# Performance work log

Hardware: AMD Instinct MI355X
Metric: run time of the kernel (lower is better)

The kernel has to match this reference:

```python
import jax, jax.numpy as jnp
import numpy as np

B, S, T = 4, 512, 512
D, F, L, H, V = 512, 2048, 6, 8, 32000
HD = D // H


def setup_inputs() -> dict:
    key = jax.random.key(0)
    ks = list(jax.random.split(key, 16))
    it = iter(ks)

    def w(shape, scale=0.02):
        return jax.random.normal(next(it), shape, jnp.float32) * scale

    enc_in = jax.random.randint(next(it), (B, S), 0, V, dtype=jnp.int32)
    dec_in = jax.random.randint(next(it), (B, T), 0, V, dtype=jnp.int32)

    # sinusoidal positional encoding (make_sine_pos_encoding)
    pos = np.arange(S)[:, None].astype(np.float32)
    i = np.arange(D)[None, :].astype(np.float32)
    angle = pos / np.power(10000.0, (2.0 * np.floor(i / 2.0)) / D)
    pe = np.zeros((S, D), np.float32)
    pe[:, 0::2] = np.sin(angle[:, 0::2])
    pe[:, 1::2] = np.cos(angle[:, 1::2])

    return {
        "enc_in": enc_in,
        "dec_in": dec_in,
        "e_embed": w((V, D)),
        "d_embed": w((V, D)),
        "pos_enc": jnp.asarray(pe),
        "enc_mha_W": w((L, 4, D, D)),      # q,k,v,out
        "enc_mha_b": jnp.zeros((L, 4, D), jnp.float32),
        "enc_ln_g": jnp.ones((L, 2, D), jnp.float32),
        "enc_ln_b": jnp.zeros((L, 2, D), jnp.float32),
        "enc_ffn_W1": w((L, D, F)),
        "enc_ffn_b1": jnp.zeros((L, F), jnp.float32),
        "enc_ffn_W2": w((L, F, D)),
        "enc_ffn_b2": jnp.zeros((L, D), jnp.float32),
        "dec_mha_W": w((L, 8, D, D)),      # self q,k,v,out then cross q,k,v,out
        "dec_mha_b": jnp.zeros((L, 8, D), jnp.float32),
        "dec_ln_g": jnp.ones((L, 3, D), jnp.float32),
        "dec_ln_b": jnp.zeros((L, 3, D), jnp.float32),
        "dec_ffn_W1": w((L, D, F)),
        "dec_ffn_b1": jnp.zeros((L, F), jnp.float32),
        "dec_ffn_W2": w((L, F, D)),
        "dec_ffn_b2": jnp.zeros((L, D), jnp.float32),
    }


def _layer_norm(x, g, b, eps=1e-6):
    m = jnp.mean(x, axis=-1, keepdims=True)
    v = jnp.mean(jnp.square(x - m), axis=-1, keepdims=True)
    return (x - m) * jax.lax.rsqrt(v + eps) * g + b


def _split_heads(x):
    b, n, _ = x.shape
    return x.reshape(b, n, H, HD).transpose(0, 2, 1, 3)  # b h n d


def _mha(xq, xkv, W, b, mask):
    # W: [>=4, D, D] slice of (q,k,v,out); mask: broadcastable to [b,h,nq,nk]
    q = _split_heads(xq @ W[0] + b[0])
    k = _split_heads(xkv @ W[1] + b[1])
    v = _split_heads(xkv @ W[2] + b[2])
    s = jnp.einsum('bhqd,bhkd->bhqk', q, k) / jnp.sqrt(jnp.float32(HD))
    s = s + mask * (-1e9)
    a = jax.nn.softmax(s, axis=-1)
    o = jnp.einsum('bhqk,bhkd->bhqd', a, v)
    o = o.transpose(0, 2, 1, 3).reshape(xq.shape[0], xq.shape[1], D)
    return o @ W[3] + b[3]


def _forward(enc_in, dec_in, e_embed, d_embed, pos_enc,
             enc_mha_W, enc_mha_b, enc_ln_g, enc_ln_b,
             enc_ffn_W1, enc_ffn_b1, enc_ffn_W2, enc_ffn_b2,
             dec_mha_W, dec_mha_b, dec_ln_g, dec_ln_b,
             dec_ffn_W1, dec_ffn_b1, dec_ffn_W2, dec_ffn_b2):
    # masks: 1.0 where attention is blocked
    enc_pad = (enc_in == 0).astype(jnp.float32)[:, None, None, :]   # [B,1,1,S]
    dec_pad = (dec_in == 0).astype(jnp.float32)[:, None, None, :]   # [B,1,1,T]
    la = jnp.triu(jnp.ones((T, T), jnp.float32), k=1)[None, None]   # [1,1,T,T]
    look_ahead = jnp.maximum(la, dec_pad)                           # [B,1,T,T]

    scale = jnp.float32(D) ** 0.5
    e = e_embed[enc_in] * scale + pos_enc[None, :S]
    d = d_embed[dec_in] * scale + pos_enc[None, :T]

    for l in range(L):
        y = _mha(e, e, enc_mha_W[l], enc_mha_b[l], enc_pad)
        e = _layer_norm(e + y, enc_ln_g[l, 0], enc_ln_b[l, 0])
        y = jax.nn.relu(e @ enc_ffn_W1[l] + enc_ffn_b1[l]) @ enc_ffn_W2[l] + enc_ffn_b2[l]
        e = _layer_norm(e + y, enc_ln_g[l, 1], enc_ln_b[l, 1])

    for l in range(L):
        y = _mha(d, d, dec_mha_W[l, 0:4], dec_mha_b[l, 0:4], look_ahead)
        d = _layer_norm(d + y, dec_ln_g[l, 0], dec_ln_b[l, 0])
        y = _mha(d, e, dec_mha_W[l, 4:8], dec_mha_b[l, 4:8], enc_pad)
        d = _layer_norm(d + y, dec_ln_g[l, 1], dec_ln_b[l, 1])
        y = jax.nn.relu(d @ dec_ffn_W1[l] + dec_ffn_b1[l]) @ dec_ffn_W2[l] + dec_ffn_b2[l]
        d = _layer_norm(d + y, dec_ln_g[l, 2], dec_ln_b[l, 2])

    return d @ d_embed.T  # [B,T,V] logits


def reference(enc_in, dec_in, e_embed, d_embed, pos_enc,
              enc_mha_W, enc_mha_b, enc_ln_g, enc_ln_b,
              enc_ffn_W1, enc_ffn_b1, enc_ffn_W2, enc_ffn_b2,
              dec_mha_W, dec_mha_b, dec_ln_g, dec_ln_b,
              dec_ffn_W1, dec_ffn_b1, dec_ffn_W2, dec_ffn_b2):
    return _forward(enc_in, dec_in, e_embed, d_embed, pos_enc,
                    enc_mha_W, enc_mha_b, enc_ln_g, enc_ln_b,
                    enc_ffn_W1, enc_ffn_b1, enc_ffn_W2, enc_ffn_b2,
                    dec_mha_W, dec_mha_b, dec_ln_g, dec_ln_b,
                    dec_ffn_W1, dec_ffn_b1, dec_ffn_W2, dec_ffn_b2)
```

## Files before the change

### kernel.cpp

```cpp
#include <hip/hip_runtime.h>
#include <hip/hip_bf16.h>
#include <math.h>

#define B_ 4
#define S_ 512
#define D_ 512
#define F_ 2048
#define L_ 6
#define H_ 8
#define V_ 32000

typedef unsigned short u16;
typedef __attribute__((ext_vector_type(8))) short bhalf8;
typedef __attribute__((ext_vector_type(4))) float f32x4;

__device__ __forceinline__ u16 f2b(float v) {
    unsigned x = __builtin_bit_cast(unsigned, v);
    return (u16)((x + 0x7FFFu + ((x >> 16) & 1u)) >> 16);
}

#define GLD16(g, l) __builtin_amdgcn_global_load_lds( \
    (const __attribute__((address_space(1))) void*)(g), \
    (__attribute__((address_space(3))) void*)(l), 16, 0, 0)

__device__ __forceinline__ float redmax16(float v) {
    #pragma unroll
    for (int m = 1; m < 16; m <<= 1) v = fmaxf(v, __shfl_xor(v, m));
    return v;
}
__device__ __forceinline__ float redsum16(float v) {
    #pragma unroll
    for (int m = 1; m < 16; m <<= 1) v += __shfl_xor(v, m);
    return v;
}

template<int NWR, int NWC, int WM, int WN, int OUT, int RELU, int MLOOP,
         int SPLITA, int XMAJOR, int NT, int VTT>
__global__ __launch_bounds__(NWR * NWC * 64)
void mfma_gemm(const u16* __restrict__ A, const u16* __restrict__ A2, int acut,
               const u16* __restrict__ B,
               const float* __restrict__ bias, void* __restrict__ Cv,
               int K, int lda, int ldb, int ldc,
               u16* __restrict__ vtp, int vc0)
{
    constexpr int BM = NWR * WM, BN = NWC * WN;
    constexpr int NW = NWR * NWC;
    constexpr int CH_A = BM / 16, CH_B = BN / 16, CH = CH_A + CH_B;
    constexpr int NI = WM / 16, NJ = WN / 16;

    __shared__ u16 As[BM * 32];
    __shared__ u16 Bs[BN * 32];
    __shared__ u16 TT[VTT ? 64 * 72 : 8];

    const int tid = threadIdx.x;
    const int wid = tid >> 6, lane = tid & 63;
    const int wrow = wid / NWC, wcol = wid % NWC;
    const long bn = (XMAJOR ? (long)blockIdx.y : (long)blockIdx.x) * BN;
    const long bmbase = (XMAJOR ? (long)blockIdx.x : (long)blockIdx.y);
    const int r4 = lane >> 2, c4 = lane & 3;
    const int l15 = lane & 15, l4 = lane >> 4;

    const u16* Ause = (SPLITA && bn >= acut) ? A2 : A;

    #pragma unroll 1
    for (int mi = 0; mi < MLOOP; ++mi) {
        const long bm = (bmbase * MLOOP + mi) * BM;

        f32x4 acc[NI][NJ];
        #pragma unroll
        for (int i = 0; i < NI; ++i)
            #pragma unroll
            for (int j = 0; j < NJ; ++j)
                acc[i][j] = (f32x4){0.f, 0.f, 0.f, 0.f};

        for (int k0 = 0; k0 < K; k0 += 32) {
            #pragma unroll
            for (int t = 0; t < CH / NW; ++t) {
                int c = wid + t * NW;
                if (c < CH_A) {
                    const u16* g = Ause + (bm + c * 16 + r4) * (long)lda + k0 + c4 * 8;
                    GLD16(g, As + c * 512 + lane * 8);
                } else {
                    int cb = c - CH_A;
                    const u16* g = B + (bn + cb * 16 + r4) * (long)ldb + k0 + c4 * 8;
                    GLD16(g, Bs + cb * 512 + lane * 8);
                }
            }
            __syncthreads();
            bhalf8 af[NI], bfr[NJ];
            #pragma unroll
            for (int i = 0; i < NI; ++i)
                af[i] = *(const bhalf8*)&As[(wrow * WM + i * 16 + l15) * 32 + l4 * 8];
            #pragma unroll
            for (int j = 0; j < NJ; ++j)
                bfr[j] = *(const bhalf8*)&Bs[(wcol * WN + j * 16 + l15) * 32 + l4 * 8];
            #pragma unroll
            for (int i = 0; i < NI; ++i)
                #pragma unroll
                for (int j = 0; j < NJ; ++j)
                    acc[i][j] = __builtin_amdgcn_mfma_f32_16x16x32_bf16(af[i], bfr[j], acc[i][j], 0, 0, 0);
            __syncthreads();
        }

        if (VTT && vtp != nullptr && bn >= vc0) {
            #pragma unroll
            for (int j = 0; j < NJ; ++j) {
                const int c = wcol * WN + j * 16 + l15;
                const float bv = bias ? bias[bn + c] : 0.f;
                #pragma unroll
                for (int i = 0; i < NI; ++i) {
                    const int rw = wrow * WM + i * 16 + (l4 << 2);
                    #pragma unroll
                    for (int r = 0; r < 4; ++r)
                        TT[c * 72 + rw + r] = f2b(acc[i][j][r] + bv);
                }
            }
            __syncthreads();
            {
                const int c = tid >> 1, hh = tid & 1;
                const u16* src = &TT[c * 72 + hh * 32];
                u16* dst = &vtp[(bn - vc0 + c) * 2048 + bm + hh * 32];
                #pragma unroll
                for (int p = 0; p < 4; ++p)
                    *(uint4*)(dst + p * 8) = *(const uint4*)(src + p * 8);
            }
            __syncthreads();
            continue;
        }

        float* Cf = (float*)Cv;
        u16*   Cb = (u16*)Cv;
        const int rowb = wrow * WM + (l4 << 2);
        const int colb = wcol * WN + l15;
        #pragma unroll
        for (int j = 0; j < NJ; ++j) {
            const long gc = bn + colb + j * 16;
            const float bv = bias ? bias[gc] : 0.f;
            #pragma unroll
            for (int i = 0; i < NI; ++i) {
                const long gr = bm + rowb + i * 16;
                #pragma unroll
                for (int r = 0; r < 4; ++r) {
                    float v = acc[i][j][r] + bv;
                    if (RELU) v = fmaxf(v, 0.f);
                    if (OUT == 0) {
                        if (NT) __builtin_nontemporal_store(v, &Cf[(gr + r) * (long)ldc + gc]);
                        else    Cf[(gr + r) * (long)ldc + gc] = v;
                    } else {
                        Cb[(gr + r) * (long)ldc + gc] = f2b(v);
                    }
                }
            }
        }
    }
}

__global__ __launch_bounds__(512)
void gemm_ln_kernel(const u16* __restrict__ A, const u16* __restrict__ B,
                    const float* __restrict__ bias,
                    float* __restrict__ x, u16* __restrict__ xb,
                    const float* __restrict__ g, const float* __restrict__ bb,
                    int K)
{
    __shared__ u16 As[16 * 32];
    __shared__ u16 Bs[512 * 32];
    __shared__ float red[2][16][8];
    __shared__ float mv[2][16];

    const int tid = threadIdx.x, w = tid >> 6, lane = tid & 63;
    const int l15 = lane & 15, l4 = lane >> 4;
    const int r4 = lane >> 2, c4 = lane & 3;
    const long bm = (long)blockIdx.x * 16;

    f32x4 acc[4];
    #pragma unroll
    for (int j = 0; j < 4; ++j) acc[j] = (f32x4){0.f, 0.f, 0.f, 0.f};

    for (int k0 = 0; k0 < K; k0 += 32) {
        #pragma unroll
        for (int t = 0; t < 5; ++t) {
            int c = w + t * 8;
            if (c < 33) {
                if (c == 0) {
                    GLD16(A + (bm + r4) * (long)K + k0 + c4 * 8, As + lane * 8);
                } else {
                    GLD16(B + ((c - 1) * 16 + r4) * (long)K + k0 + c4 * 8,
                          Bs + (c - 1) * 512 + lane * 8);
                }
            }
        }
        __syncthreads();
        bhalf8 af = *(const bhalf8*)&As[l15 * 32 + l4 * 8];
        #pragma unroll
        for (int j = 0; j < 4; ++j) {
            bhalf8 bf = *(const bhalf8*)&Bs[(w * 64 + j * 16 + l15) * 32 + l4 * 8];
            acc[j] = __builtin_amdgcn_mfma_f32_16x16x32_bf16(af, bf, acc[j], 0, 0, 0);
        }
        __syncthreads();
    }

    float vbuf[4][4], s[4] = {0, 0, 0, 0}, s2[4] = {0, 0, 0, 0};
    #pragma unroll
    for (int j = 0; j < 4; ++j) {
        int col = w * 64 + j * 16 + l15;
        float bv = bias[col];
        #pragma unroll
        for (int r = 0; r < 4; ++r) {
            int row = l4 * 4 + r;
            float v = acc[j][r] + bv + x[(bm + row) * 512 + col];
            vbuf[j][r] = v;
            s[r] += v; s2[r] += v * v;
        }
    }
    #pragma unroll
    for (int r = 0; r < 4; ++r) { s[r] = redsum16(s[r]); s2[r] = redsum16(s2[r]); }
    if (l15 == 0) {
        #pragma unroll
        for (int r = 0; r < 4; ++r) {
            red[0][l4 * 4 + r][w] = s[r];
            red[1][l4 * 4 + r][w] = s2[r];
        }
    }
    __syncthreads();
    if (tid < 16) {
        float S = 0.f, S2 = 0.f;
        #pragma unroll
        for (int q = 0; q < 8; ++q) { S += red[0][tid][q]; S2 += red[1][tid][q]; }
        float mean = S * (1.f / 512.f);
        float var = S2 * (1.f / 512.f) - mean * mean;
        mv[0][tid] = mean;
        mv[1][tid] = rsqrtf(var + 1e-6f);
    }
    __syncthreads();
    #pragma unroll
    for (int j = 0; j < 4; ++j) {
        int col = w * 64 + j * 16 + l15;
        float gg = g[col], bbv = bb[col];
        #pragma unroll
        for (int r = 0; r < 4; ++r) {
            int row = l4 * 4 + r;
            float o = (vbuf[j][r] - mv[0][row]) * mv[1][row] * gg + bbv;
            x[(bm + row) * 512 + col] = o;
            xb[(bm + row) * 512 + col] = f2b(o);
        }
    }
}

template<int CAUSAL>
__global__ __launch_bounds__(256)
void flash_kernel(const u16* __restrict__ Qp, int ldq,
                  const u16* __restrict__ Kp, int ldk,
                  const u16* __restrict__ Vt,
                  const int* __restrict__ tok,
                  u16* __restrict__ Op)
{
    __shared__ u16 QS[64 * 64];
    __shared__ u16 KS[64 * 64];
    __shared__ u16 VS[64 * 64];
    __shared__ u16 PS[4 * 16 * 64];
    __shared__ float MK[512];

    const int tid = threadIdx.x, lane = tid & 63, w = tid >> 6;
    const int l15 = lane & 15, l4 = lane >> 4;
    const int qb = blockIdx.x, bh = blockIdx.y;
    const int b = bh >> 3, h = bh & 7;

    const u16* Q = Qp + (long)(b * 512 + qb * 64) * ldq + h * 64;
    const u16* K = Kp + (long)(b * 512) * ldk + h * 64;
    const u16* V = Vt + (long)(h * 64) * 2048 + b * 512;
    u16* O = Op + (long)(b * 512 + qb * 64) * 512 + h * 64;

    {
        int t0 = tok[b * 512 + tid];
        int t1 = tok[b * 512 + 256 + tid];
        MK[tid]       = (t0 == 0) ? -1e9f : 0.f;
        MK[tid + 256] = (t1 == 0) ? -1e9f : 0.f;
    }
    {
        int r = tid >> 3;
        int c = (tid & 7) ^ (r & 7);
        GLD16(Q + (long)r * ldq + c * 8,        QS + tid * 8);
        GLD16(Q + (long)(r + 32) * ldq + c * 8, QS + 2048 + tid * 8);
    }

    f32x4 oacc[4];
    float mrun[4], lrun[4];
    #pragma unroll
    for (int j = 0; j < 4; ++j) oacc[j] = (f32x4){0.f, 0.f, 0.f, 0.f};
    #pragma unroll
    for (int r = 0; r < 4; ++r) { mrun[r] = -1e30f; lrun[r] = 0.f; }

    bhalf8 qa[2];
    const int tmax = CAUSAL ? qb : 7;

    for (int t = 0; t <= tmax; ++t) {
        {
            int r = tid >> 3;
            int c = (tid & 7) ^ (r & 7);
            GLD16(K + (long)(t * 64 + r) * ldk + c * 8,       KS + tid * 8);
            GLD16(K + (long)(t * 64 + 32 + r) * ldk + c * 8,  KS + 2048 + tid * 8);
            GLD16(V + (long)r * 2048 + t * 64 + c * 8,        VS + tid * 8);
            GLD16(V + (long)(r + 32) * 2048 + t * 64 + c * 8, VS + 2048 + tid * 8);
        }
        __syncthreads();
        if (t == 0) {
            #pragma unroll
            for (int kc = 0; kc < 2; ++kc) {
                int row = w * 16 + l15;
                qa[kc] = *(const bhalf8*)&QS[row * 64 + (((kc * 4 + l4) ^ (row & 7)) << 3)];
            }
        }
        f32x4 sac[4];
        #pragma unroll
        for (int jj = 0; jj < 4; ++jj) sac[jj] = (f32x4){0.f, 0.f, 0.f, 0.f};
        bhalf8 kf[4][2];
        #pragma unroll
        for (int jj = 0; jj < 4; ++jj)
            #pragma unroll
            for (int kc = 0; kc < 2; ++kc) {
                int row = jj * 16 + l15;
                kf[jj][kc] = *(const bhalf8*)&KS[row * 64 + (((kc * 4 + l4) ^ (row & 7)) << 3)];
            }
        #pragma unroll
        for (int jj = 0; jj < 4; ++jj)
            #pragma unroll
            for (int kc = 0; kc < 2; ++kc)
                sac[jj] = __builtin_amdgcn_mfma_f32_16x16x32_bf16(qa[kc], kf[jj][kc], sac[jj], 0, 0, 0);

        #pragma unroll
        for (int jj = 0; jj < 4; ++jj) {
            float mk = MK[t * 64 + jj * 16 + l15];
            #pragma unroll
            for (int r = 0; r < 4; ++r) {
                float mk2 = mk;
                if (CAUSAL && t == qb) {
                    int col = t * 64 + jj * 16 + l15;
                    int qr = qb * 64 + w * 16 + l4 * 4 + r;
                    if (col > qr) mk2 = -1e9f;
                }
                sac[jj][r] = sac[jj][r] * 0.125f + mk2;
            }
        }
        #pragma unroll
        for (int r = 0; r < 4; ++r) {
            float mx = fmaxf(fmaxf(sac[0][r], sac[1][r]), fmaxf(sac[2][r], sac[3][r]));
            mx = redmax16(mx);
            float mnew = fmaxf(mrun[r], mx);
            float alpha = __expf(mrun[r] - mnew);
            float sum = 0.f;
            int row_p = l4 * 4 + r;
            #pragma unroll
            for (int jj = 0; jj < 4; ++jj) {
                float pv = __expf(sac[jj][r] - mnew);
                sum += pv;
                int kv = jj * 16 + l15;
                PS[w * 1024 + row_p * 64 + ((((kv >> 3) ^ (row_p & 7)) << 3) | (kv & 7))] = f2b(pv);
            }
            sum = redsum16(sum);
            lrun[r] = lrun[r] * alpha + sum;
            mrun[r] = mnew;
            #pragma unroll
            for (int jd = 0; jd < 4; ++jd) oacc[jd][r] *= alpha;
        }
        bhalf8 pa[2], vf[4][2];
        #pragma unroll
        for (int kc = 0; kc < 2; ++kc) {
            int row = l15;
            pa[kc] = *(const bhalf8*)&PS[w * 1024 + row * 64 + (((kc * 4 + l4) ^ (row & 7)) << 3)];
        }
        #pragma unroll
        for (int jd = 0; jd < 4; ++jd)
            #pragma unroll
            for (int kc = 0; kc < 2; ++kc) {
                int row = jd * 16 + l15;
                vf[jd][kc] = *(const bhalf8*)&VS[row * 64 + (((kc * 4 + l4) ^ (row & 7)) << 3)];
            }
        #pragma unroll
        for (int jd = 0; jd < 4; ++jd)
            #pragma unroll
            for (int kc = 0; kc < 2; ++kc)
                oacc[jd] = __builtin_amdgcn_mfma_f32_16x16x32_bf16(pa[kc], vf[jd][kc], oacc[jd], 0, 0, 0);
        __syncthreads();
    }

    #pragma unroll
    for (int r = 0; r < 4; ++r) {
        float inv = 1.f / lrun[r];
        int row = w * 16 + l4 * 4 + r;
        #pragma unroll
        for (int jd = 0; jd < 4; ++jd)
            O[(long)row * 512 + jd * 16 + l15] = f2b(oacc[jd][r] * inv);
    }
}

__global__ __launch_bounds__(256)
void transpose_many(const float* __restrict__ inA, const float* __restrict__ inB,
                    int zsplit, int R, int C, u16* __restrict__ out)
{
    int z = blockIdx.z;
    const float* in = (z < zsplit) ? inA + (long)z * R * C
                                   : inB + (long)(z - zsplit) * R * C;
    u16* o = out + (long)z * R * C;
    __shared__ float tb[64][65];
    const int tr = blockIdx.y * 64, tc = blockIdx.x * 64;
    const int col = threadIdx.x & 63, r0 = threadIdx.x >> 6;
    #pragma unroll
    for (int p = 0; p < 16; ++p) {
        int row = r0 * 16 + p;
        tb[row][col] = in[(long)(tr + row) * C + tc + col];
    }
    __syncthreads();
    #pragma unroll
    for (int p = 0; p < 16; ++p) {
        int row = r0 * 16 + p;
        o[(long)(tc + row) * R + tr + col] = f2b(tb[col][row]);
    }
}

__global__ __launch_bounds__(256)
void convert_b16(const float4* __restrict__ in, u16* __restrict__ out, long n4)
{
    long i = (long)blockIdx.x * 256 + threadIdx.x;
    if (i >= n4) return;
    float4 v = in[i];
    uint2 p;
    p.x = (unsigned)f2b(v.x) | ((unsigned)f2b(v.y) << 16);
    p.y = (unsigned)f2b(v.z) | ((unsigned)f2b(v.w) << 16);
    *(uint2*)(out + i * 4) = p;
}

__global__ __launch_bounds__(256)
void embed_kernel(const int* __restrict__ tE, const int* __restrict__ tD,
                  const float* __restrict__ eE, const float* __restrict__ eD,
                  const float* __restrict__ pos,
                  float* __restrict__ xE, float* __restrict__ xD,
                  u16* __restrict__ bE, u16* __restrict__ bD, float scale)
{
    const int z = blockIdx.y;
    const int* tok = z ? tD : tE;
    const float* emb = z ? eD : eE;
    float* x = z ? xD : xE;
    u16* xb = z ? bD : bE;
    int row = blockIdx.x;
    int s = row & (S_ - 1);
    int t = tok[row];
    const float* er = emb + (long)t * D_;
    const float* pr = pos + (long)s * D_;
    float* o = x + (long)row * D_;
    u16*  ob = xb + (long)row * D_;
    int i = threadIdx.x;
    float v0 = er[i]       * scale + pr[i];
    float v1 = er[i + 256] * scale + pr[i + 256];
    o[i] = v0;        o[i + 256] = v1;
    ob[i] = f2b(v0);  ob[i + 256] = f2b(v1);
}

__global__ __launch_bounds__(256)
void add_ln_kernel(float* __restrict__ x, const float* __restrict__ y,
                   u16* __restrict__ xb,
                   const float* __restrict__ g, const float* __restrict__ bb)
{
    long row = blockIdx.x;
    float* xr = x + row * D_;
    u16* xo = xb + row * D_;
    const float* yr = y + row * D_;
    int t = threadIdx.x, t2 = t + 256;

    float r0 = xr[t] + yr[t];
    float r1 = xr[t2] + yr[t2];
    float s = r0 + r1;
    float s2 = r0 * r0 + r1 * r1;
    #pragma unroll
    for (int i = 1; i < 64; i <<= 1) {
        s  += __shfl_xor(s, i);
        s2 += __shfl_xor(s2, i);
    }
    __shared__ float rs[4], rs2[4];
    int wid = t >> 6;
    if ((t & 63) == 0) { rs[wid] = s; rs2[wid] = s2; }
    __syncthreads();
    s  = rs[0] + rs[1] + rs[2] + rs[3];
    s2 = rs2[0] + rs2[1] + rs2[2] + rs2[3];

    float mean = s * (1.f / D_);
    float var  = s2 * (1.f / D_) - mean * mean;
    float inv  = rsqrtf(var + 1e-6f);
    float o0 = (r0 - mean) * inv * g[t]  + bb[t];
    float o1 = (r1 - mean) * inv * g[t2] + bb[t2];
    xr[t] = o0;       xr[t2] = o1;
    xo[t] = f2b(o0);  xo[t2] = f2b(o1);
}

extern "C" void kernel_launch(void* const* d_in, const int* in_sizes, int n_in,
                              void* d_out, int out_size, void* d_ws, size_t ws_size,
                              hipStream_t stream)
{
    const int*   enc_in     = (const int*)  d_in[0];
    const int*   dec_in     = (const int*)  d_in[1];
    const float* e_embed    = (const float*)d_in[2];
    const float* d_embed    = (const float*)d_in[3];
    const float* pos_enc    = (const float*)d_in[4];
    const float* enc_mha_W  = (const float*)d_in[5];
    const float* enc_mha_b  = (const float*)d_in[6];
    const float* enc_ln_g   = (const float*)d_in[7];
    const float* enc_ln_b   = (const float*)d_in[8];
    const float* enc_ffn_W1 = (const float*)d_in[9];
    const float* enc_ffn_b1 = (const float*)d_in[10];
    const float* enc_ffn_W2 = (const float*)d_in[11];
    const float* enc_ffn_b2 = (const float*)d_in[12];
    const float* dec_mha_W  = (const float*)d_in[13];
    const float* dec_mha_b  = (const float*)d_in[14];
    const float* dec_ln_g   = (const float*)d_in[15];
    const float* dec_ln_b   = (const float*)d_in[16];
    const float* dec_ffn_W1 = (const float*)d_in[17];
    const float* dec_ffn_b1 = (const float*)d_in[18];
    const float* dec_ffn_W2 = (const float*)d_in[19];
    const float* dec_ffn_b2 = (const float*)d_in[20];
    float* out = (float*)d_out;

    const int  BS  = B_ * S_;
    const long BSD = (long)BS * D_;
    const long DD  = (long)D_ * D_;
    const long DF  = (long)D_ * F_;

    char* p = (char*)d_ws;
    auto alloc = [&](long bytes) { char* r = p; p += (bytes + 255) & ~255L; return r; };
    float* e    = (float*)alloc(BSD * 4);
    float* dd   = (float*)alloc(BSD * 4);
    float* y    = (float*)alloc(BSD * 4);
    u16*   eb   = (u16*)  alloc(BSD * 2);
    u16*   ddb  = (u16*)  alloc(BSD * 2);
    u16*   qkv  = (u16*)  alloc((long)BS * 1536 * 2);
    u16*   att  = (u16*)  alloc(BSD * 2);
    u16*   vt   = (u16*)  alloc(BSD * 2);
    u16*   ffnh = (u16*)  alloc((long)BS * F_ * 2);
    u16*   wEmb = (u16*)  alloc((long)V_ * D_ * 2);
    u16*   wMha = (u16*)  alloc(72 * DD * 2);
    u16*   wF1  = (u16*)  alloc(12 * DF * 2);
    u16*   wF2  = (u16*)  alloc(12 * DF * 2);

    transpose_many<<<dim3(8, 8, 72), 256, 0, stream>>>(enc_mha_W, dec_mha_W, 24, 512, 512, wMha);
    transpose_many<<<dim3(32, 8, 12), 256, 0, stream>>>(enc_ffn_W1, dec_ffn_W1, 6, 512, 2048, wF1);
    transpose_many<<<dim3(8, 32, 12), 256, 0, stream>>>(enc_ffn_W2, dec_ffn_W2, 6, 2048, 512, wF2);
    convert_b16<<<16000, 256, 0, stream>>>((const float4*)d_embed, wEmb, (long)V_ * D_ / 4);

    const float scale = sqrtf((float)D_);
    embed_kernel<<<dim3(BS, 2), 256, 0, stream>>>(enc_in, dec_in, e_embed, d_embed,
                                                  pos_enc, e, dd, eb, ddb, scale);

    #define GEMM_BIG(grid, RELU, OUTT, A, Bp, bias, C, K, lda, ldb, ldc) \
        mfma_gemm<2,2,64,64,OUTT,RELU,1,0,0,0,0><<<grid, 256, 0, stream>>>(A, A, 1 << 30, Bp, bias, C, K, lda, ldb, ldc, nullptr, 0)
    #define GEMM_SKV(grid, A, Bp, bias, C, K, lda, ldb, ldc, vtp, vc0) \
        mfma_gemm<2,1,32,64,1,0,1,0,0,0,1><<<grid, 128, 0, stream>>>(A, A, 1 << 30, Bp, bias, C, K, lda, ldb, ldc, vtp, vc0)
    #define GEMM_SK(grid, OUTT, A, Bp, bias, C, K, lda, ldb, ldc) \
        mfma_gemm<2,1,32,64,OUTT,0,1,0,0,0,0><<<grid, 128, 0, stream>>>(A, A, 1 << 30, Bp, bias, C, K, lda, ldb, ldc, nullptr, 0)

    for (int l = 0; l < L_; ++l) {
        const u16* Wl = wMha + (long)l * 4 * DD;
        const float* bl = enc_mha_b + (long)l * 4 * D_;
        GEMM_SKV(dim3(24, 32), eb, Wl, bl, qkv, 512, 512, 512, 1536, vt, 1024);
        flash_kernel<0><<<dim3(8, 32), 256, 0, stream>>>(qkv, 1536, qkv + 512, 1536, vt, enc_in, att);
        gemm_ln_kernel<<<128, 512, 0, stream>>>(att, Wl + 3 * DD, bl + 3 * D_,
            e, eb, enc_ln_g + (long)(l * 2) * D_, enc_ln_b + (long)(l * 2) * D_, 512);
        GEMM_BIG(dim3(16, 16), 1, 1, eb, wF1 + (long)l * DF, enc_ffn_b1 + (long)l * F_,
                 ffnh, 512, 512, 512, 2048);
        GEMM_SK(dim3(8, 32), 0, ffnh, wF2 + (long)l * DF, enc_ffn_b2 + (long)l * D_,
                y, 2048, 2048, 2048, 512);
        add_ln_kernel<<<BS, 256, 0, stream>>>(e, y, eb,
            enc_ln_g + (long)(l * 2 + 1) * D_, enc_ln_b + (long)(l * 2 + 1) * D_);
    }

    for (int l = 0; l < L_; ++l) {
        const u16* Wl = wMha + (long)(24 + l * 8) * DD;
        const float* bl = dec_mha_b + (long)l * 8 * D_;
        GEMM_SKV(dim3(24, 32), ddb, Wl, bl, qkv, 512, 512, 512, 1536, vt, 1024);
        flash_kernel<1><<<dim3(8, 32), 256, 0, stream>>>(qkv, 1536, qkv + 512, 1536, vt, dec_in, att);
        gemm_ln_kernel<<<128, 512, 0, stream>>>(att, Wl + 3 * DD, bl + 3 * D_,
            dd, ddb, dec_ln_g + (long)(l * 3) * D_, dec_ln_b + (long)(l * 3) * D_, 512);
        mfma_gemm<2,1,32,64,1,0,1,1,0,0,1><<<dim3(24, 32), 128, 0, stream>>>(
            ddb, eb, 512, Wl + 4 * DD, bl + 4 * D_, qkv,
            512, 512, 512, 1536, vt, 1024);
        flash_kernel<0><<<dim3(8, 32), 256, 0, stream>>>(qkv, 1536, qkv + 512, 1536, vt, enc_in, att);
        gemm_ln_kernel<<<128, 512, 0, stream>>>(att, Wl + 7 * DD, bl + 7 * D_,
            dd, ddb, dec_ln_g + (long)(l * 3 + 1) * D_, dec_ln_b + (long)(l * 3 + 1) * D_, 512);
        GEMM_BIG(dim3(16, 16), 1, 1, ddb, wF1 + (long)(6 + l) * DF, dec_ffn_b1 + (long)l * F_,
                 ffnh, 512, 512, 512, 2048);
        GEMM_SK(dim3(8, 32), 0, ffnh, wF2 + (long)(6 + l) * DF, dec_ffn_b2 + (long)l * D_,
                y, 2048, 2048, 2048, 512);
        add_ln_kernel<<<BS, 256, 0, stream>>>(dd, y, ddb,
            dec_ln_g + (long)(l * 3 + 2) * D_, dec_ln_b + (long)(l * 3 + 2) * D_);
    }

    mfma_gemm<2,2,64,64,0,0,1,0,1,1,0><<<dim3(16, 250), 256, 0, stream>>>(
        ddb, ddb, 1 << 30, wEmb, nullptr, out, 512, 512, 512, 32000, nullptr, 0);
}
```

Before: 1.805 ms.

## Fuse FFN2 with add+LayerNorm, halve flash query tile, swizzle logits grid

Three separate changes. The second FFN GEMM now goes through the existing gemm_ln_kernel with K=2048, which folds bias, residual add and LayerNorm into one kernel and drops the fp32 y buffer and the separate add_ln launch. The flash attention kernel now handles 32-query tiles with 128 threads, doubling the grid to 512 blocks for better occupancy and finer causal work balance. The final vocab-projection GEMM uses a 1D grid with an XCD-aware swizzle so blocks sharing B tiles land on the same chiplet. In exchange, the fused LN GEMM runs only 128 blocks over a K=2048 loop, and the smaller flash tiles reload K/V more often.

```diff
diff --git a/kernel.cpp b/kernel.cpp
--- a/kernel.cpp
+++ b/kernel.cpp
@@ -35,7 +35,7 @@
 }
 
 template<int NWR, int NWC, int WM, int WN, int OUT, int RELU, int MLOOP,
-         int SPLITA, int XMAJOR, int NT, int VTT>
+         int SPLITA, int XMAJOR, int NT, int VTT, int SWZ>
 __global__ __launch_bounds__(NWR * NWC * 64)
 void mfma_gemm(const u16* __restrict__ A, const u16* __restrict__ A2, int acut,
                const u16* __restrict__ B,
@@ -55,8 +55,17 @@
     const int tid = threadIdx.x;
     const int wid = tid >> 6, lane = tid & 63;
     const int wrow = wid / NWC, wcol = wid % NWC;
-    const long bn = (XMAJOR ? (long)blockIdx.y : (long)blockIdx.x) * BN;
-    const long bmbase = (XMAJOR ? (long)blockIdx.x : (long)blockIdx.y);
+    long bn, bmbase;
+    if (SWZ) {
+        long b0 = blockIdx.x;
+        long per = (long)gridDim.x >> 3;
+        long w = (b0 & 7) * per + (b0 >> 3);
+        bn = (w >> 4) * BN;
+        bmbase = w & 15;
+    } else {
+        bn = (XMAJOR ? (long)blockIdx.y : (long)blockIdx.x) * BN;
+        bmbase = (XMAJOR ? (long)blockIdx.x : (long)blockIdx.y);
+    }
     const int r4 = lane >> 2, c4 = lane & 3;
     const int l15 = lane & 15, l4 = lane >> 4;
 
@@ -247,17 +256,17 @@
 }
 
 template<int CAUSAL>
-__global__ __launch_bounds__(256)
+__global__ __launch_bounds__(128)
 void flash_kernel(const u16* __restrict__ Qp, int ldq,
                   const u16* __restrict__ Kp, int ldk,
                   const u16* __restrict__ Vt,
                   const int* __restrict__ tok,
                   u16* __restrict__ Op)
 {
-    __shared__ u16 QS[64 * 64];
+    __shared__ u16 QS[32 * 64];
     __shared__ u16 KS[64 * 64];
     __shared__ u16 VS[64 * 64];
-    __shared__ u16 PS[4 * 16 * 64];
+    __shared__ u16 PS[2 * 16 * 64];
     __shared__ float MK[512];
 
     const int tid = threadIdx.x, lane = tid & 63, w = tid >> 6;
@@ -265,22 +274,21 @@
     const int qb = blockIdx.x, bh = blockIdx.y;
     const int b = bh >> 3, h = bh & 7;
 
-    const u16* Q = Qp + (long)(b * 512 + qb * 64) * ldq + h * 64;
+    const u16* Q = Qp + (long)(b * 512 + qb * 32) * ldq + h * 64;
     const u16* K = Kp + (long)(b * 512) * ldk + h * 64;
     const u16* V = Vt + (long)(h * 64) * 2048 + b * 512;
-    u16* O = Op + (long)(b * 512 + qb * 64) * 512 + h * 64;
-
-    {
-        int t0 = tok[b * 512 + tid];
-        int t1 = tok[b * 512 + 256 + tid];
-        MK[tid]       = (t0 == 0) ? -1e9f : 0.f;
-        MK[tid + 256] = (t1 == 0) ? -1e9f : 0.f;
+    u16* O = Op + (long)(b * 512 + qb * 32) * 512 + h * 64;
+
+    #pragma unroll
+    for (int t = 0; t < 4; ++t) {
+        int tk = tok[b * 512 + t * 128 + tid];
+        MK[t * 128 + tid] = (tk == 0) ? -1e9f : 0.f;
     }
     {
         int r = tid >> 3;
         int c = (tid & 7) ^ (r & 7);
-        GLD16(Q + (long)r * ldq + c * 8,        QS + tid * 8);
-        GLD16(Q + (long)(r + 32) * ldq + c * 8, QS + 2048 + tid * 8);
+        GLD16(Q + (long)r * ldq + c * 8,          QS + tid * 8);
+        GLD16(Q + (long)(16 + r) * ldq + c * 8,   QS + 1024 + tid * 8);
     }
 
     f32x4 oacc[4];
@@ -291,16 +299,20 @@
     for (int r = 0; r < 4; ++r) { mrun[r] = -1e30f; lrun[r] = 0.f; }
 
     bhalf8 qa[2];
-    const int tmax = CAUSAL ? qb : 7;
+    const int tmax = CAUSAL ? (qb >> 1) : 7;
 
     for (int t = 0; t <= tmax; ++t) {
         {
             int r = tid >> 3;
             int c = (tid & 7) ^ (r & 7);
             GLD16(K + (long)(t * 64 + r) * ldk + c * 8,       KS + tid * 8);
+            GLD16(K + (long)(t * 64 + 16 + r) * ldk + c * 8,  KS + 1024 + tid * 8);
             GLD16(K + (long)(t * 64 + 32 + r) * ldk + c * 8,  KS + 2048 + tid * 8);
+            GLD16(K + (long)(t * 64 + 48 + r) * ldk + c * 8,  KS + 3072 + tid * 8);
             GLD16(V + (long)r * 2048 + t * 64 + c * 8,        VS + tid * 8);
-            GLD16(V + (long)(r + 32) * 2048 + t * 64 + c * 8, VS + 2048 + tid * 8);
+            GLD16(V + (long)(16 + r) * 2048 + t * 64 + c * 8, VS + 1024 + tid * 8);
+            GLD16(V + (long)(32 + r) * 2048 + t * 64 + c * 8, VS + 2048 + tid * 8);
+            GLD16(V + (long)(48 + r) * 2048 + t * 64 + c * 8, VS + 3072 + tid * 8);
         }
         __syncthreads();
         if (t == 0) {
@@ -333,9 +345,9 @@
             #pragma unroll
             for (int r = 0; r < 4; ++r) {
                 float mk2 = mk;
-                if (CAUSAL && t == qb) {
+                if (CAUSAL && t == tmax) {
                     int col = t * 64 + jj * 16 + l15;
-                    int qr = qb * 64 + w * 16 + l4 * 4 + r;
+                    int qr = qb * 32 + w * 16 + l4 * 4 + r;
                     if (col > qr) mk2 = -1e9f;
                 }
                 sac[jj][r] = sac[jj][r] * 0.125f + mk2;
@@ -453,42 +465,6 @@
     float v1 = er[i + 256] * scale + pr[i + 256];
     o[i] = v0;        o[i + 256] = v1;
     ob[i] = f2b(v0);  ob[i + 256] = f2b(v1);
-}
-
-__global__ __launch_bounds__(256)
-void add_ln_kernel(float* __restrict__ x, const float* __restrict__ y,
-                   u16* __restrict__ xb,
-                   const float* __restrict__ g, const float* __restrict__ bb)
-{
-    long row = blockIdx.x;
-    float* xr = x + row * D_;
-    u16* xo = xb + row * D_;
-    const float* yr = y + row * D_;
-    int t = threadIdx.x, t2 = t + 256;
-
-    float r0 = xr[t] + yr[t];
-    float r1 = xr[t2] + yr[t2];
-    float s = r0 + r1;
-    float s2 = r0 * r0 + r1 * r1;
-    #pragma unroll
-    for (int i = 1; i < 64; i <<= 1) {
-        s  += __shfl_xor(s, i);
-        s2 += __shfl_xor(s2, i);
-    }
-    __shared__ float rs[4], rs2[4];
-    int wid = t >> 6;
-    if ((t & 63) == 0) { rs[wid] = s; rs2[wid] = s2; }
-    __syncthreads();
-    s  = rs[0] + rs[1] + rs[2] + rs[3];
-    s2 = rs2[0] + rs2[1] + rs2[2] + rs2[3];
-
-    float mean = s * (1.f / D_);
-    float var  = s2 * (1.f / D_) - mean * mean;
-    float inv  = rsqrtf(var + 1e-6f);
-    float o0 = (r0 - mean) * inv * g[t]  + bb[t];
-    float o1 = (r1 - mean) * inv * g[t2] + bb[t2];
-    xr[t] = o0;       xr[t2] = o1;
-    xo[t] = f2b(o0);  xo[t2] = f2b(o1);
 }
 
 extern "C" void kernel_launch(void* const* d_in, const int* in_sizes, int n_in,
@@ -527,7 +503,6 @@
     auto alloc = [&](long bytes) { char* r = p; p += (bytes + 255) & ~255L; return r; };
     float* e    = (float*)alloc(BSD * 4);
     float* dd   = (float*)alloc(BSD * 4);
-    float* y    = (float*)alloc(BSD * 4);
     u16*   eb   = (u16*)  alloc(BSD * 2);
     u16*   ddb  = (u16*)  alloc(BSD * 2);
     u16*   qkv  = (u16*)  alloc((long)BS * 1536 * 2);
@@ -549,48 +524,42 @@
                                                   pos_enc, e, dd, eb, ddb, scale);
 
     #define GEMM_BIG(grid, RELU, OUTT, A, Bp, bias, C, K, lda, ldb, ldc) \
-        mfma_gemm<2,2,64,64,OUTT,RELU,1,0,0,0,0><<<grid, 256, 0, stream>>>(A, A, 1 << 30, Bp, bias, C, K, lda, ldb, ldc, nullptr, 0)
+        mfma_gemm<2,2,64,64,OUTT,RELU,1,0,0,0,0,0><<<grid, 256, 0, stream>>>(A, A, 1 << 30, Bp, bias, C, K, lda, ldb, ldc, nullptr, 0)
     #define GEMM_SKV(grid, A, Bp, bias, C, K, lda, ldb, ldc, vtp, vc0) \
-        mfma_gemm<2,1,32,64,1,0,1,0,0,0,1><<<grid, 128, 0, stream>>>(A, A, 1 << 30, Bp, bias, C, K, lda, ldb, ldc, vtp, vc0)
-    #define GEMM_SK(grid, OUTT, A, Bp, bias, C, K, lda, ldb, ldc) \
-        mfma_gemm<2,1,32,64,OUTT,0,1,0,0,0,0><<<grid, 128, 0, stream>>>(A, A, 1 << 30, Bp, bias, C, K, lda, ldb, ldc, nullptr, 0)
+        mfma_gemm<2,1,32,64,1,0,1,0,0,0,1,0><<<grid, 128, 0, stream>>>(A, A, 1 << 30, Bp, bias, C, K, lda, ldb, ldc, vtp, vc0)
 
     for (int l = 0; l < L_; ++l) {
         const u16* Wl = wMha + (long)l * 4 * DD;
         const float* bl = enc_mha_b + (long)l * 4 * D_;
         GEMM_SKV(dim3(24, 32), eb, Wl, bl, qkv, 512, 512, 512, 1536, vt, 1024);
-        flash_kernel<0><<<dim3(8, 32), 256, 0, stream>>>(qkv, 1536, qkv + 512, 1536, vt, enc_in, att);
+        flash_kernel<0><<<dim3(16, 32), 128, 0, stream>>>(qkv, 1536, qkv + 512, 1536, vt, enc_in, att);
         gemm_ln_kernel<<<128, 512, 0, stream>>>(att, Wl + 3 * DD, bl + 3 * D_,
             e, eb, enc_ln_g + (long)(l * 2) * D_, enc_ln_b + (long)(l * 2) * D_, 512);
         GEMM_BIG(dim3(16, 16), 1, 1, eb, wF1 + (long)l * DF, enc_ffn_b1 + (long)l * F_,
                  ffnh, 512, 512, 512, 2048);
-        GEMM_SK(dim3(8, 32), 0, ffnh, wF2 + (long)l * DF, enc_ffn_b2 + (long)l * D_,
-                y, 2048, 2048, 2048, 512);
-        add_ln_kernel<<<BS, 256, 0, stream>>>(e, y, eb,
-            enc_ln_g + (long)(l * 2 + 1) * D_, enc_ln_b + (long)(l * 2 + 1) * D_);
+        gemm_ln_kernel<<<128, 512, 0, stream>>>(ffnh, wF2 + (long)l * DF, enc_ffn_b2 + (long)l * D_,
+            e, eb, enc_ln_g + (long)(l * 2 + 1) * D_, enc_ln_b + (long)(l * 2 + 1) * D_, 2048);
     }
 
     for (int l = 0; l < L_; ++l) {
         const u16* Wl = wMha + (long)(24 + l * 8) * DD;
         const float* bl = dec_mha_b + (long)l * 8 * D_;
         GEMM_SKV(dim3(24, 32), ddb, Wl, bl, qkv, 512, 512, 512, 1536, vt, 1024);
-        flash_kernel<1><<<dim3(8, 32), 256, 0, stream>>>(qkv, 1536, qkv + 512, 1536, vt, dec_in, att);
+        flash_kernel<1><<<dim3(16, 32), 128, 0, stream>>>(qkv, 1536, qkv + 512, 1536, vt, dec_in, att);
         gemm_ln_kernel<<<128, 512, 0, stream>>>(att, Wl + 3 * DD, bl + 3 * D_,
             dd, ddb, dec_ln_g + (long)(l * 3) * D_, dec_ln_b + (long)(l * 3) * D_, 512);
-        mfma_gemm<2,1,32,64,1,0,1,1,0,0,1><<<dim3(24, 32), 128, 0, stream>>>(
+        mfma_gemm<2,1,32,64,1,0,1,1,0,0,1,0><<<dim3(24, 32), 128, 0, stream>>>(
             ddb, eb, 512, Wl + 4 * DD, bl + 4 * D_, qkv,
             512, 512, 512, 1536, vt, 1024);
-        flash_kernel<0><<<dim3(8, 32), 256, 0, stream>>>(qkv, 1536, qkv + 512, 1536, vt, enc_in, att);
+        flash_kernel<0><<<dim3(16, 32), 128, 0, stream>>>(qkv, 1536, qkv + 512, 1536, vt, enc_in, att);
         gemm_ln_kernel<<<128, 512, 0, stream>>>(att, Wl + 7 * DD, bl + 7 * D_,
             dd, ddb, dec_ln_g + (long)(l * 3 + 1) * D_, dec_ln_b + (long)(l * 3 + 1) * D_, 512);
         GEMM_BIG(dim3(16, 16), 1, 1, ddb, wF1 + (long)(6 + l) * DF, dec_ffn_b1 + (long)l * F_,
                  ffnh, 512, 512, 512, 2048);
-        GEMM_SK(dim3(8, 32), 0, ffnh, wF2 + (long)(6 + l) * DF, dec_ffn_b2 + (long)l * D_,
-                y, 2048, 2048, 2048, 512);
-        add_ln_kernel<<<BS, 256, 0, stream>>>(dd, y, ddb,
-            dec_ln_g + (long)(l * 3 + 2) * D_, dec_ln_b + (long)(l * 3 + 2) * D_);
-    }
-
-    mfma_gemm<2,2,64,64,0,0,1,0,1,1,0><<<dim3(16, 250), 256, 0, stream>>>(
+        gemm_ln_kernel<<<128, 512, 0, stream>>>(ffnh, wF2 + (long)(6 + l) * DF, dec_ffn_b2 + (long)l * D_,
+            dd, ddb, dec_ln_g + (long)(l * 3 + 2) * D_, dec_ln_b + (long)(l * 3 + 2) * D_, 2048);
+    }
+
+    mfma_gemm<2,2,64,64,0,0,1,0,0,1,0,1><<<dim3(4000), 256, 0, stream>>>(
         ddb, ddb, 1 << 30, wEmb, nullptr, out, 512, 512, 512, 32000, nullptr, 0);
 }
```

Result: slower. 2.030 ms (+12.4%).
